# Kernel tuning notes

Measured on AMD Instinct MI355X. Metric: run time of the kernel, lower is better.

The kernel has to match this reference:

```python
import jax, jax.numpy as jnp
import numpy as np

R_EARTH = 6371000.0


def _time_derivative(f, dt):
    # f: (b, t, ...); central differences interior, one-sided at ends (dim 1)
    return jnp.concatenate([
        (f[:, 1:2] - f[:, 0:1]) / dt,
        (f[:, 2:] - f[:, :-2]) / (2.0 * dt),
        (f[:, -1:] - f[:, -2:-1]) / dt,
    ], axis=1)


def _space_derivatives(x, lat, dx, dy):
    # x: (..., H, W); lat: (H,) degrees. Returns (d/dlat, d/dlon) in 1/m.
    m_per_lat = jnp.pi * R_EARTH / 180.0                      # scalar (const over lat)
    m_per_lon = m_per_lat * jnp.cos(lat * jnp.pi / 180.0)     # (H,)
    ady = dy * m_per_lat                                      # scalar meters
    adx = (dx * m_per_lon)[:, None]                           # (H, 1), broadcasts over W
    der_lat = jnp.concatenate([
        (x[..., 1:2, :] - x[..., 0:1, :]) / ady,
        (x[..., 2:, :] - x[..., :-2, :]) / (2.0 * ady),
        (x[..., -1:, :] - x[..., -2:-1, :]) / ady,
    ], axis=-2)
    der_lon = jnp.concatenate([
        (x[..., :, 1:2] - x[..., :, 0:1]),
        (x[..., :, 2:] - x[..., :, :-2]) / 2.0,
        (x[..., :, -1:] - x[..., :, -2:-1]),
    ], axis=-1) / adx
    return der_lat, der_lon


def _residual(u, v, sp, lat, atmos_levels, dt, dx, dy):
    # u, v: (b, t, c, h, w); sp: (b, t, h, w)
    log_sp = jnp.log(sp)
    dlog_sp_dt = _time_derivative(log_sp, dt)                         # (b,t,h,w)
    _, du_dx = _space_derivatives(u, lat, dx, dy)
    dv_dy, _ = _space_derivatives(v, lat, dx, dy)
    dlsp_dy, dlsp_dx = _space_derivatives(log_sp, lat, dx, dy)        # (b,t,h,w)
    advection = u * dlsp_dx[:, :, None] + v * dlsp_dy[:, :, None]     # (b,t,c,h,w)
    total_effect = du_dx + dv_dy + advection
    # sigma layer thickness
    p_levels = (atmos_levels * 100.0)[None, None, :, None, None]      # Pa, (1,1,c,1,1)
    sigma = p_levels / sp[:, :, None]                                 # (b,t,c,h,w)
    delta_sigma = jnp.concatenate([
        sigma[:, :, 1:2] - sigma[:, :, 0:1],
        (sigma[:, :, 2:] - sigma[:, :, :-2]) / 2.0,
        sigma[:, :, -1:] - sigma[:, :, -2:-1],
    ], axis=2)
    integrated = jnp.sum(total_effect * delta_sigma, axis=2)          # (b,t,h,w)
    # residual = dlog_sp_dt - rhs, rhs = -integrated
    return dlog_sp_dt + integrated


def setup_inputs() -> dict:
    key = jax.random.key(0)
    ks = jax.random.split(key, 6)
    b, t, c, h, w = 1, 4, 13, 361, 720
    shape5 = (b, t, c, h, w)
    preds_u = 10.0 * jax.random.normal(ks[0], shape5, dtype=jnp.float32)
    preds_v = 10.0 * jax.random.normal(ks[1], shape5, dtype=jnp.float32)
    target_u = 10.0 * jax.random.normal(ks[2], shape5, dtype=jnp.float32)
    target_v = 10.0 * jax.random.normal(ks[3], shape5, dtype=jnp.float32)
    # surface pressure ~ 1e5 Pa, strictly positive for log()
    preds_sp = 101325.0 * (1.0 + 0.02 * jax.random.normal(ks[4], (b, t, h, w), dtype=jnp.float32))
    target_sp = 101325.0 * (1.0 + 0.02 * jax.random.normal(ks[5], (b, t, h, w), dtype=jnp.float32))
    lat = jnp.linspace(90.0, -90.0, h, dtype=jnp.float32)
    atmos_levels = jnp.array([50, 100, 150, 200, 250, 300, 400, 500, 600, 700, 850, 925, 1000], dtype=jnp.float32)
    return {
        "preds_u": preds_u, "preds_v": preds_v, "preds_sp": preds_sp,
        "target_u": target_u, "target_v": target_v, "target_sp": target_sp,
        "lat": lat, "atmos_levels": atmos_levels,
        "dt": jnp.float32(6.0), "dx": jnp.float32(0.5), "dy": jnp.float32(0.5),
    }


def reference(preds_u, preds_v, preds_sp, target_u, target_v, target_sp, lat, atmos_levels, dt, dx, dy):
    era5_res = _residual(target_u, target_v, target_sp, lat, atmos_levels, dt, dx, dy)
    model_res = _residual(preds_u, preds_v, preds_sp, lat, atmos_levels, dt, dx, dy)
    return jnp.mean(jnp.square(model_res - era5_res))
```

## Files before the change

kernel.cpp:

```cpp
#include <hip/hip_runtime.h>
#include <math.h>

#define B_ 1
#define T_ 4
#define C_ 13
#define H_ 361
#define W_ 720
constexpr int HW   = H_ * W_;
constexpr int N4   = T_ * HW;
constexpr int W4   = W_ / 4;
constexpr int NTHR1 = T_ * H_ * W4;
constexpr int BLK  = 256;
constexpr int GRID2 = (N4 + BLK - 1) / BLK;

constexpr size_t PART_OFF_BYTES = (size_t)(6 * N4 + 362) * 4;

__global__ __launch_bounds__(BLK) void k1_reduce(
    const float* __restrict__ pu, const float* __restrict__ pv,
    const float* __restrict__ psp,
    const float* __restrict__ tu, const float* __restrict__ tv,
    const float* __restrict__ tsp,
    const float* __restrict__ lat, const float* __restrict__ lev,
    const float* __restrict__ dxp,
    float* __restrict__ ws)
{
    const int idx = blockIdx.x * BLK + threadIdx.x;

    if (idx < H_) {
        const float m_per_lat = (float)(M_PI * 6371000.0 / 180.0);
        float ang = (lat[idx] * (float)M_PI) / 180.0f;
        float c   = (float)cos((double)ang);
        ws[6 * N4 + idx] = dxp[0] * (m_per_lat * c);
    }
    if (idx >= NTHR1) return;

    const int t   = idx / (H_ * W4);
    const int rem = idx - t * (H_ * W4);
    const int base5 = t * (C_ * HW) + rem * 4;
    const int base4 = t * HW + rem * 4;

    float p[C_];
#pragma unroll
    for (int c = 0; c < C_; ++c) p[c] = lev[c] * 100.0f;
    float dp[C_];
    dp[0] = p[1] - p[0];
    dp[C_ - 1] = p[C_ - 1] - p[C_ - 2];
#pragma unroll
    for (int c = 1; c < C_ - 1; ++c) dp[c] = (p[c + 1] - p[c - 1]) * 0.5f;

    float4 sup = {0.f, 0.f, 0.f, 0.f}, svp = sup, sut = sup, svt = sup;
#pragma unroll
    for (int c = 0; c < C_; ++c) {
        const int o = base5 + c * HW;
        const float wgt = dp[c];
        float4 a = *(const float4*)(pu + o);
        float4 b = *(const float4*)(pv + o);
        float4 x = *(const float4*)(tu + o);
        float4 y = *(const float4*)(tv + o);
        sup.x = fmaf(wgt, a.x, sup.x); sup.y = fmaf(wgt, a.y, sup.y);
        sup.z = fmaf(wgt, a.z, sup.z); sup.w = fmaf(wgt, a.w, sup.w);
        svp.x = fmaf(wgt, b.x, svp.x); svp.y = fmaf(wgt, b.y, svp.y);
        svp.z = fmaf(wgt, b.z, svp.z); svp.w = fmaf(wgt, b.w, svp.w);
        sut.x = fmaf(wgt, x.x, sut.x); sut.y = fmaf(wgt, x.y, sut.y);
        sut.z = fmaf(wgt, x.z, sut.z); sut.w = fmaf(wgt, x.w, sut.w);
        svt.x = fmaf(wgt, y.x, svt.x); svt.y = fmaf(wgt, y.y, svt.y);
        svt.z = fmaf(wgt, y.z, svt.z); svt.w = fmaf(wgt, y.w, svt.w);
    }

    float4 sa = *(const float4*)(psp + base4);
    float4 sb = *(const float4*)(tsp + base4);
    float4 la = {logf(sa.x), logf(sa.y), logf(sa.z), logf(sa.w)};
    float4 lb = {logf(sb.x), logf(sb.y), logf(sb.z), logf(sb.w)};

    *(float4*)(ws + 0 * N4 + base4) = sup;
    *(float4*)(ws + 1 * N4 + base4) = svp;
    *(float4*)(ws + 2 * N4 + base4) = sut;
    *(float4*)(ws + 3 * N4 + base4) = svt;
    *(float4*)(ws + 4 * N4 + base4) = la;
    *(float4*)(ws + 5 * N4 + base4) = lb;
}

__device__ __forceinline__ float residual_at(
    const float* __restrict__ U, const float* __restrict__ V,
    const float* __restrict__ L, const float* __restrict__ sp,
    int n, int t, int h, int w, float dt, float ady, float ax)
{
    float dLdt;
    if (t == 0)            dLdt = (L[n + HW] - L[n]) / dt;
    else if (t == T_ - 1)  dLdt = (L[n] - L[n - HW]) / dt;
    else                   dLdt = (L[n + HW] - L[n - HW]) / (2.0f * dt);

    float dLdy, dVdy;
    if (h == 0)            { dLdy = (L[n + W_] - L[n]) / ady;  dVdy = (V[n + W_] - V[n]) / ady; }
    else if (h == H_ - 1)  { dLdy = (L[n] - L[n - W_]) / ady;  dVdy = (V[n] - V[n - W_]) / ady; }
    else {
        dLdy = (L[n + W_] - L[n - W_]) / (2.0f * ady);
        dVdy = (V[n + W_] - V[n - W_]) / (2.0f * ady);
    }

    float dLdx, dUdx;
    if (w == 0)            { dLdx = (L[n + 1] - L[n]) / ax;  dUdx = (U[n + 1] - U[n]) / ax; }
    else if (w == W_ - 1)  { dLdx = (L[n] - L[n - 1]) / ax;  dUdx = (U[n] - U[n - 1]) / ax; }
    else {
        dLdx = ((L[n + 1] - L[n - 1]) * 0.5f) / ax;
        dUdx = ((U[n + 1] - U[n - 1]) * 0.5f) / ax;
    }

    float s = sp[n];
    float integ = (dUdx + dVdy + U[n] * dLdx + V[n] * dLdy) / s;
    return dLdt + integ;
}

__global__ __launch_bounds__(BLK) void k2_stencil(
    const float* __restrict__ psp, const float* __restrict__ tsp,
    const float* __restrict__ ws,
    const float* __restrict__ dtp, const float* __restrict__ dyp,
    double* __restrict__ part)
{
    const int n = blockIdx.x * BLK + threadIdx.x;
    double val = 0.0;
    if (n < N4) {
        const int t = n / HW;
        const int rem = n - t * HW;
        const int h = rem / W_;
        const int w = rem - h * W_;

        const float* Up = ws;
        const float* Vp = ws + 1 * N4;
        const float* Ut = ws + 2 * N4;
        const float* Vt = ws + 3 * N4;
        const float* Lp = ws + 4 * N4;
        const float* Lt = ws + 5 * N4;
        const float* adx = ws + 6 * N4;

        const float dt = dtp[0];
        const float m_per_lat = (float)(M_PI * 6371000.0 / 180.0);
        const float ady = dyp[0] * m_per_lat;
        const float ax = adx[h];

        float rm = residual_at(Up, Vp, Lp, psp, n, t, h, w, dt, ady, ax);
        float re = residual_at(Ut, Vt, Lt, tsp, n, t, h, w, dt, ady, ax);
        float d = rm - re;
        val = (double)d * (double)d;
    }

    for (int o = 32; o > 0; o >>= 1) val += __shfl_down(val, o, 64);
    __shared__ double lds[BLK / 64];
    const int lane = threadIdx.x & 63;
    const int wid  = threadIdx.x >> 6;
    if (lane == 0) lds[wid] = val;
    __syncthreads();
    if (threadIdx.x == 0) {
        double s = lds[0] + lds[1] + lds[2] + lds[3];
        part[blockIdx.x] = s;
    }
}

__global__ __launch_bounds__(BLK) void k3_final(
    const double* __restrict__ part, float* __restrict__ out)
{
    double v = 0.0;
    for (int i = threadIdx.x; i < GRID2; i += BLK) v += part[i];
    for (int o = 32; o > 0; o >>= 1) v += __shfl_down(v, o, 64);
    __shared__ double lds[BLK / 64];
    const int lane = threadIdx.x & 63;
    const int wid  = threadIdx.x >> 6;
    if (lane == 0) lds[wid] = v;
    __syncthreads();
    if (threadIdx.x == 0) {
        double s = lds[0] + lds[1] + lds[2] + lds[3];
        out[0] = (float)(s / (double)N4);
    }
}

extern "C" void kernel_launch(void* const* d_in, const int* in_sizes, int n_in,
                              void* d_out, int out_size, void* d_ws, size_t ws_size,
                              hipStream_t stream)
{
    const float* pu  = (const float*)d_in[0];
    const float* pv  = (const float*)d_in[1];
    const float* psp = (const float*)d_in[2];
    const float* tu  = (const float*)d_in[3];
    const float* tv  = (const float*)d_in[4];
    const float* tsp = (const float*)d_in[5];
    const float* lat = (const float*)d_in[6];
    const float* lev = (const float*)d_in[7];
    const float* dtp = (const float*)d_in[8];
    const float* dxp = (const float*)d_in[9];
    const float* dyp = (const float*)d_in[10];

    float*  ws   = (float*)d_ws;
    double* part = (double*)((char*)d_ws + PART_OFF_BYTES);

    const int g1 = (NTHR1 + BLK - 1) / BLK;
    hipLaunchKernelGGL(k1_reduce, dim3(g1), dim3(BLK), 0, stream,
                       pu, pv, psp, tu, tv, tsp, lat, lev, dxp, ws);
    hipLaunchKernelGGL(k2_stencil, dim3(GRID2), dim3(BLK), 0, stream,
                       psp, tsp, ws, dtp, dyp, part);
    hipLaunchKernelGGL(k3_final, dim3(1), dim3(BLK), 0, stream,
                       part, (float*)d_out);
}
```

Before: 249.6 us.

## Split level reduction across tensors and vectorize stencil to four points per thread

The level-reduction kernel now uses a second grid dimension so each block handles one of the four u/v tensors. All 13 level loads are issued up front, which spreads memory traffic over four times as many blocks. The stencil kernel now computes four adjacent points per thread with float4 loads for the center, vertical and time neighbours, plus scalar halo loads at the edges. This cuts per-point index math and redundant neighbour loads, at the cost of more register use and more complex boundary handling.

```diff
diff --git a/kernel.cpp b/kernel.cpp
--- a/kernel.cpp
+++ b/kernel.cpp
@@ -1,19 +1,22 @@
 #include <hip/hip_runtime.h>
 #include <math.h>
 
-#define B_ 1
 #define T_ 4
 #define C_ 13
 #define H_ 361
 #define W_ 720
-constexpr int HW   = H_ * W_;
-constexpr int N4   = T_ * HW;
-constexpr int W4   = W_ / 4;
+constexpr int HW    = H_ * W_;
+constexpr int N4    = T_ * HW;
+constexpr int W4    = W_ / 4;
 constexpr int NTHR1 = T_ * H_ * W4;
-constexpr int BLK  = 256;
-constexpr int GRID2 = (N4 + BLK - 1) / BLK;
+constexpr int BLK   = 256;
+constexpr int G1    = (NTHR1 + BLK - 1) / BLK;
+constexpr int NTHR2 = N4 / 4;
+constexpr int G2    = (NTHR2 + BLK - 1) / BLK;
 
 constexpr size_t PART_OFF_BYTES = (size_t)(6 * N4 + 362) * 4;
+
+__device__ __forceinline__ float4 ld4(const float* p) { return *(const float4*)p; }
 
 __global__ __launch_bounds__(BLK) void k1_reduce(
     const float* __restrict__ pu, const float* __restrict__ pv,
@@ -24,9 +27,10 @@
     const float* __restrict__ dxp,
     float* __restrict__ ws)
 {
+    const int tensor = blockIdx.y;
     const int idx = blockIdx.x * BLK + threadIdx.x;
 
-    if (idx < H_) {
+    if (tensor == 2 && idx < H_) {
         const float m_per_lat = (float)(M_PI * 6371000.0 / 180.0);
         float ang = (lat[idx] * (float)M_PI) / 180.0f;
         float c   = (float)cos((double)ang);
@@ -34,81 +38,110 @@
     }
     if (idx >= NTHR1) return;
 
-    const int t   = idx / (H_ * W4);
-    const int rem = idx - t * (H_ * W4);
+    const int t    = idx / (H_ * W4);
+    const int rem  = idx - t * (H_ * W4);
     const int base5 = t * (C_ * HW) + rem * 4;
     const int base4 = t * HW + rem * 4;
 
-    float p[C_];
-#pragma unroll
-    for (int c = 0; c < C_; ++c) p[c] = lev[c] * 100.0f;
     float dp[C_];
-    dp[0] = p[1] - p[0];
-    dp[C_ - 1] = p[C_ - 1] - p[C_ - 2];
-#pragma unroll
-    for (int c = 1; c < C_ - 1; ++c) dp[c] = (p[c + 1] - p[c - 1]) * 0.5f;
-
-    float4 sup = {0.f, 0.f, 0.f, 0.f}, svp = sup, sut = sup, svt = sup;
+    {
+        float p[C_];
+#pragma unroll
+        for (int c = 0; c < C_; ++c) p[c] = lev[c] * 100.0f;
+        dp[0] = p[1] - p[0];
+        dp[C_ - 1] = p[C_ - 1] - p[C_ - 2];
+#pragma unroll
+        for (int c = 1; c < C_ - 1; ++c) dp[c] = (p[c + 1] - p[c - 1]) * 0.5f;
+    }
+
+    const float* src = (tensor == 0) ? pu : (tensor == 1) ? pv : (tensor == 2) ? tu : tv;
+
+    float4 v[C_];
+#pragma unroll
+    for (int c = 0; c < C_; ++c) v[c] = ld4(src + base5 + c * HW);
+
+    float4 acc = {0.f, 0.f, 0.f, 0.f};
 #pragma unroll
     for (int c = 0; c < C_; ++c) {
-        const int o = base5 + c * HW;
-        const float wgt = dp[c];
-        float4 a = *(const float4*)(pu + o);
-        float4 b = *(const float4*)(pv + o);
-        float4 x = *(const float4*)(tu + o);
-        float4 y = *(const float4*)(tv + o);
-        sup.x = fmaf(wgt, a.x, sup.x); sup.y = fmaf(wgt, a.y, sup.y);
-        sup.z = fmaf(wgt, a.z, sup.z); sup.w = fmaf(wgt, a.w, sup.w);
-        svp.x = fmaf(wgt, b.x, svp.x); svp.y = fmaf(wgt, b.y, svp.y);
-        svp.z = fmaf(wgt, b.z, svp.z); svp.w = fmaf(wgt, b.w, svp.w);
-        sut.x = fmaf(wgt, x.x, sut.x); sut.y = fmaf(wgt, x.y, sut.y);
-        sut.z = fmaf(wgt, x.z, sut.z); sut.w = fmaf(wgt, x.w, sut.w);
-        svt.x = fmaf(wgt, y.x, svt.x); svt.y = fmaf(wgt, y.y, svt.y);
-        svt.z = fmaf(wgt, y.z, svt.z); svt.w = fmaf(wgt, y.w, svt.w);
-    }
-
-    float4 sa = *(const float4*)(psp + base4);
-    float4 sb = *(const float4*)(tsp + base4);
-    float4 la = {logf(sa.x), logf(sa.y), logf(sa.z), logf(sa.w)};
-    float4 lb = {logf(sb.x), logf(sb.y), logf(sb.z), logf(sb.w)};
-
-    *(float4*)(ws + 0 * N4 + base4) = sup;
-    *(float4*)(ws + 1 * N4 + base4) = svp;
-    *(float4*)(ws + 2 * N4 + base4) = sut;
-    *(float4*)(ws + 3 * N4 + base4) = svt;
-    *(float4*)(ws + 4 * N4 + base4) = la;
-    *(float4*)(ws + 5 * N4 + base4) = lb;
-}
-
-__device__ __forceinline__ float residual_at(
+        acc.x = fmaf(dp[c], v[c].x, acc.x);
+        acc.y = fmaf(dp[c], v[c].y, acc.y);
+        acc.z = fmaf(dp[c], v[c].z, acc.z);
+        acc.w = fmaf(dp[c], v[c].w, acc.w);
+    }
+    *(float4*)(ws + (size_t)tensor * N4 + base4) = acc;
+
+    if (tensor == 0) {
+        float4 s4 = ld4(psp + base4);
+        float4 l4 = {logf(s4.x), logf(s4.y), logf(s4.z), logf(s4.w)};
+        *(float4*)(ws + 4 * N4 + base4) = l4;
+    } else if (tensor == 1) {
+        float4 s4 = ld4(tsp + base4);
+        float4 l4 = {logf(s4.x), logf(s4.y), logf(s4.z), logf(s4.w)};
+        *(float4*)(ws + 5 * N4 + base4) = l4;
+    }
+}
+
+__device__ __forceinline__ void resid4(
     const float* __restrict__ U, const float* __restrict__ V,
     const float* __restrict__ L, const float* __restrict__ sp,
-    int n, int t, int h, int w, float dt, float ady, float ax)
-{
-    float dLdt;
-    if (t == 0)            dLdt = (L[n + HW] - L[n]) / dt;
-    else if (t == T_ - 1)  dLdt = (L[n] - L[n - HW]) / dt;
-    else                   dLdt = (L[n + HW] - L[n - HW]) / (2.0f * dt);
-
-    float dLdy, dVdy;
-    if (h == 0)            { dLdy = (L[n + W_] - L[n]) / ady;  dVdy = (V[n + W_] - V[n]) / ady; }
-    else if (h == H_ - 1)  { dLdy = (L[n] - L[n - W_]) / ady;  dVdy = (V[n] - V[n - W_]) / ady; }
-    else {
-        dLdy = (L[n + W_] - L[n - W_]) / (2.0f * ady);
-        dVdy = (V[n + W_] - V[n - W_]) / (2.0f * ady);
-    }
-
-    float dLdx, dUdx;
-    if (w == 0)            { dLdx = (L[n + 1] - L[n]) / ax;  dUdx = (U[n + 1] - U[n]) / ax; }
-    else if (w == W_ - 1)  { dLdx = (L[n] - L[n - 1]) / ax;  dUdx = (U[n] - U[n - 1]) / ax; }
-    else {
-        dLdx = ((L[n + 1] - L[n - 1]) * 0.5f) / ax;
-        dUdx = ((U[n + 1] - U[n - 1]) * 0.5f) / ax;
-    }
-
-    float s = sp[n];
-    float integ = (dUdx + dVdy + U[n] * dLdx + V[n] * dLdy) / s;
-    return dLdt + integ;
+    int n, int t, int h, int w4, float dt, float ady, float ax,
+    float out[4])
+{
+    float4 Uc4 = ld4(U + n), Vc4 = ld4(V + n), Lc4 = ld4(L + n), S4 = ld4(sp + n);
+    const int up = (h > 0)      ? n - W_ : n;
+    const int dn = (h < H_ - 1) ? n + W_ : n;
+    float4 Vu4 = ld4(V + up), Vd4 = ld4(V + dn);
+    float4 Lu4 = ld4(L + up), Ld4 = ld4(L + dn);
+    float4 Lp4 = (t > 0)      ? ld4(L + n - HW) : Lc4;
+    float4 Ln4 = (t < T_ - 1) ? ld4(L + n + HW) : Lc4;
+    float Ul = (w4 > 0)      ? U[n - 1] : 0.f;
+    float Ur = (w4 < W4 - 1) ? U[n + 4] : 0.f;
+    float Ll = (w4 > 0)      ? L[n - 1] : 0.f;
+    float Lr = (w4 < W4 - 1) ? L[n + 4] : 0.f;
+
+    const float Uc[4] = {Uc4.x, Uc4.y, Uc4.z, Uc4.w};
+    const float Vc[4] = {Vc4.x, Vc4.y, Vc4.z, Vc4.w};
+    const float Lc[4] = {Lc4.x, Lc4.y, Lc4.z, Lc4.w};
+    const float S[4]  = {S4.x,  S4.y,  S4.z,  S4.w};
+    const float Vu[4] = {Vu4.x, Vu4.y, Vu4.z, Vu4.w};
+    const float Vd[4] = {Vd4.x, Vd4.y, Vd4.z, Vd4.w};
+    const float Lu[4] = {Lu4.x, Lu4.y, Lu4.z, Lu4.w};
+    const float Ld[4] = {Ld4.x, Ld4.y, Ld4.z, Ld4.w};
+    const float Lp[4] = {Lp4.x, Lp4.y, Lp4.z, Lp4.w};
+    const float Ln[4] = {Ln4.x, Ln4.y, Ln4.z, Ln4.w};
+
+#pragma unroll
+    for (int j = 0; j < 4; ++j) {
+        float dLdt;
+        if (t == 0)           dLdt = (Ln[j] - Lc[j]) / dt;
+        else if (t == T_ - 1) dLdt = (Lc[j] - Lp[j]) / dt;
+        else                  dLdt = (Ln[j] - Lp[j]) / (2.0f * dt);
+
+        float dLdy, dVdy;
+        if (h == 0)           { dLdy = (Ld[j] - Lc[j]) / ady; dVdy = (Vd[j] - Vc[j]) / ady; }
+        else if (h == H_ - 1) { dLdy = (Lc[j] - Lu[j]) / ady; dVdy = (Vc[j] - Vu[j]) / ady; }
+        else {
+            dLdy = (Ld[j] - Lu[j]) / (2.0f * ady);
+            dVdy = (Vd[j] - Vu[j]) / (2.0f * ady);
+        }
+
+        const float uL = (j > 0) ? Uc[j - 1] : Ul;
+        const float uR = (j < 3) ? Uc[j + 1] : Ur;
+        const float lL = (j > 0) ? Lc[j - 1] : Ll;
+        const float lR = (j < 3) ? Lc[j + 1] : Lr;
+        float dUdx, dLdx;
+        const bool at0 = (w4 == 0 && j == 0);
+        const bool atE = (w4 == W4 - 1 && j == 3);
+        if (at0)      { dUdx = (Uc[1] - Uc[0]) / ax; dLdx = (Lc[1] - Lc[0]) / ax; }
+        else if (atE) { dUdx = (Uc[3] - Uc[2]) / ax; dLdx = (Lc[3] - Lc[2]) / ax; }
+        else {
+            dUdx = ((uR - uL) * 0.5f) / ax;
+            dLdx = ((lR - lL) * 0.5f) / ax;
+        }
+
+        float integ = (dUdx + dVdy + Uc[j] * dLdx + Vc[j] * dLdy) / S[j];
+        out[j] = dLdt + integ;
+    }
 }
 
 __global__ __launch_bounds__(BLK) void k2_stencil(
@@ -117,31 +150,29 @@
     const float* __restrict__ dtp, const float* __restrict__ dyp,
     double* __restrict__ part)
 {
-    const int n = blockIdx.x * BLK + threadIdx.x;
+    const int idx = blockIdx.x * BLK + threadIdx.x;
     double val = 0.0;
-    if (n < N4) {
-        const int t = n / HW;
-        const int rem = n - t * HW;
-        const int h = rem / W_;
-        const int w = rem - h * W_;
-
-        const float* Up = ws;
-        const float* Vp = ws + 1 * N4;
-        const float* Ut = ws + 2 * N4;
-        const float* Vt = ws + 3 * N4;
-        const float* Lp = ws + 4 * N4;
-        const float* Lt = ws + 5 * N4;
+    if (idx < NTHR2) {
+        const int t   = idx / (H_ * W4);
+        const int rem = idx - t * (H_ * W4);
+        const int h   = rem / W4;
+        const int w4  = rem - h * W4;
+        const int n   = t * HW + h * W_ + w4 * 4;
+
         const float* adx = ws + 6 * N4;
-
         const float dt = dtp[0];
         const float m_per_lat = (float)(M_PI * 6371000.0 / 180.0);
         const float ady = dyp[0] * m_per_lat;
-        const float ax = adx[h];
-
-        float rm = residual_at(Up, Vp, Lp, psp, n, t, h, w, dt, ady, ax);
-        float re = residual_at(Ut, Vt, Lt, tsp, n, t, h, w, dt, ady, ax);
-        float d = rm - re;
-        val = (double)d * (double)d;
+        const float ax  = adx[h];
+
+        float rm[4], re[4];
+        resid4(ws + 0 * N4, ws + 1 * N4, ws + 4 * N4, psp, n, t, h, w4, dt, ady, ax, rm);
+        resid4(ws + 2 * N4, ws + 3 * N4, ws + 5 * N4, tsp, n, t, h, w4, dt, ady, ax, re);
+#pragma unroll
+        for (int j = 0; j < 4; ++j) {
+            float d = rm[j] - re[j];
+            val += (double)d * (double)d;
+        }
     }
 
     for (int o = 32; o > 0; o >>= 1) val += __shfl_down(val, o, 64);
@@ -150,17 +181,14 @@
     const int wid  = threadIdx.x >> 6;
     if (lane == 0) lds[wid] = val;
     __syncthreads();
-    if (threadIdx.x == 0) {
-        double s = lds[0] + lds[1] + lds[2] + lds[3];
-        part[blockIdx.x] = s;
-    }
+    if (threadIdx.x == 0) part[blockIdx.x] = lds[0] + lds[1] + lds[2] + lds[3];
 }
 
 __global__ __launch_bounds__(BLK) void k3_final(
     const double* __restrict__ part, float* __restrict__ out)
 {
     double v = 0.0;
-    for (int i = threadIdx.x; i < GRID2; i += BLK) v += part[i];
+    for (int i = threadIdx.x; i < G2; i += BLK) v += part[i];
     for (int o = 32; o > 0; o >>= 1) v += __shfl_down(v, o, 64);
     __shared__ double lds[BLK / 64];
     const int lane = threadIdx.x & 63;
@@ -192,10 +220,9 @@
     float*  ws   = (float*)d_ws;
     double* part = (double*)((char*)d_ws + PART_OFF_BYTES);
 
-    const int g1 = (NTHR1 + BLK - 1) / BLK;
-    hipLaunchKernelGGL(k1_reduce, dim3(g1), dim3(BLK), 0, stream,
+    hipLaunchKernelGGL(k1_reduce, dim3(G1, 4), dim3(BLK), 0, stream,
                        pu, pv, psp, tu, tv, tsp, lat, lev, dxp, ws);
-    hipLaunchKernelGGL(k2_stencil, dim3(GRID2), dim3(BLK), 0, stream,
+    hipLaunchKernelGGL(k2_stencil, dim3(G2), dim3(BLK), 0, stream,
                        psp, tsp, ws, dtp, dyp, part);
     hipLaunchKernelGGL(k3_final, dim3(1), dim3(BLK), 0, stream,
                        part, (float*)d_out);
```

New measurement: 243.0 us. 2.6% less time.
